# Performance work log

Hardware: AMD Instinct MI355X
Metric: run time of the kernel (lower is better)

## Reference

```python
import jax, jax.numpy as jnp
import numpy as np

DIM = 1024
NUM_HEADS = 16
HEAD_DIM = DIM // NUM_HEADS
SCALE = HEAD_DIM ** -0.5


def setup_inputs() -> dict:
    key = jax.random.key(0)
    ks = jax.random.split(key, 11)
    B, T = 2, 2048
    std = DIM ** -0.5
    return {
        "query": jax.random.normal(ks[0], (B, T, DIM), jnp.float32),
        "key": jax.random.normal(ks[1], (B, T, DIM), jnp.float32),
        "value": jax.random.normal(ks[2], (B, T, DIM), jnp.float32),
        "wq": jax.random.normal(ks[3], (DIM, DIM), jnp.float32) * std,
        "bq": jnp.zeros((DIM,), jnp.float32),
        "wk": jax.random.normal(ks[4], (DIM, DIM), jnp.float32) * std,
        "bk": jnp.zeros((DIM,), jnp.float32),
        "wv": jax.random.normal(ks[5], (DIM, DIM), jnp.float32) * std,
        "bv": jnp.zeros((DIM,), jnp.float32),
        "wo": jax.random.normal(ks[6], (DIM, DIM), jnp.float32) * std,
        "bo": jnp.zeros((DIM,), jnp.float32),
    }


def reference(query, key, value, wq, bq, wk, bk, wv, bv, wo, bo):
    B, Tq, D = query.shape
    Tk = key.shape[1]
    H, Hd = NUM_HEADS, HEAD_DIM
    # projections (torch Linear: x @ W^T + b); reshape to [B, H, T, Hd]
    q = (query @ wq.T + bq).reshape(B, Tq, H, Hd).transpose(0, 2, 1, 3)
    k = (key @ wk.T + bk).reshape(B, Tk, H, Hd).transpose(0, 2, 1, 3)
    v = (value @ wv.T + bv).reshape(B, Tk, H, Hd).transpose(0, 2, 1, 3)
    # attention scores [B, H, Tq, Tk]
    attn = jnp.einsum("bhqd,bhkd->bhqk", q, k) * SCALE
    attn = jax.nn.softmax(attn, axis=-1)
    # dropout p=0.0 -> identity
    out = jnp.einsum("bhqk,bhkd->bhqd", attn, v)
    out = out.transpose(0, 2, 1, 3).reshape(B, Tq, D)
    return out @ wo.T + bo
```

## Files before the change

kernel.cpp:

```cpp
#include <hip/hip_runtime.h>
#include <math.h>


typedef __attribute__((ext_vector_type(8))) short short8;
typedef __attribute__((ext_vector_type(4))) float f32x4;
typedef __attribute__((ext_vector_type(4))) float float4v;
typedef __attribute__((ext_vector_type(4))) unsigned short ushort4v;
typedef __attribute__((ext_vector_type(2))) unsigned int uint2v;

typedef __attribute__((address_space(3))) unsigned int lds_uint;
typedef __attribute__((address_space(1))) unsigned int glb_uint;

__device__ __forceinline__ void gload_lds16(const void* g, void* l) {
    __builtin_amdgcn_global_load_lds((glb_uint*)(unsigned long long)g,
                                     (lds_uint*)(unsigned int)(unsigned long long)l,
                                     16, 0, 0);
}

__device__ __forceinline__ unsigned short f32_bf16(float f) {
    union { float f; unsigned int u; } x; x.f = f;
    unsigned int r = x.u + 0x7fffu + ((x.u >> 16) & 1u);
    return (unsigned short)(r >> 16);
}

__device__ __forceinline__ unsigned int cvt_pk_bf16(float lo, float hi) {
    unsigned int r;
    asm("v_cvt_pk_bf16_f32 %0, %1, %2" : "=v"(r) : "v"(lo), "v"(hi));
    return r;
}

__device__ __forceinline__ float exp2_fast(float x) {
    float r;
    asm("v_exp_f32 %0, %1" : "=v"(r) : "v"(x));
    return r;
}

#define QSCALE 0.18033688011112042f

__global__ void pack3_bf16(const float* __restrict__ a, const float* __restrict__ b,
                           const float* __restrict__ c,
                           unsigned short* __restrict__ oa, unsigned short* __restrict__ ob,
                           unsigned short* __restrict__ oc, int n4) {
    const int y = blockIdx.y;
    const float* in = (y == 0) ? a : (y == 1) ? b : c;
    unsigned short* out = (y == 0) ? oa : (y == 1) ? ob : oc;
    int i = blockIdx.x * blockDim.x + threadIdx.x;
    if (i < n4) {
        float4v v = ((const float4v*)in)[i];
        ushort4v o;
        o.x = f32_bf16(v.x); o.y = f32_bf16(v.y);
        o.z = f32_bf16(v.z); o.w = f32_bf16(v.w);
        ((ushort4v*)out)[i] = o;
    }
}

__global__ void pack4_bf16(const float* __restrict__ a, const float* __restrict__ b,
                           const float* __restrict__ c, const float* __restrict__ d,
                           unsigned short* __restrict__ oa, unsigned short* __restrict__ ob,
                           unsigned short* __restrict__ oc, unsigned short* __restrict__ od,
                           int n4) {
    const int y = blockIdx.y;
    const float* in = (y == 0) ? a : (y == 1) ? b : (y == 2) ? c : d;
    unsigned short* out = (y == 0) ? oa : (y == 1) ? ob : (y == 2) ? oc : od;
    int i = blockIdx.x * blockDim.x + threadIdx.x;
    if (i < n4) {
        float4v v = ((const float4v*)in)[i];
        ushort4v o;
        o.x = f32_bf16(v.x); o.y = f32_bf16(v.y);
        o.z = f32_bf16(v.z); o.w = f32_bf16(v.w);
        ((ushort4v*)out)[i] = o;
    }
}

__global__ __launch_bounds__(256, 2) void gemm_qkv(
    const unsigned short* __restrict__ A0, const unsigned short* __restrict__ A1,
    const unsigned short* __restrict__ A2,
    const unsigned short* __restrict__ W0, const unsigned short* __restrict__ W1,
    const unsigned short* __restrict__ W2,
    const float* __restrict__ bs0, const float* __restrict__ bs1,
    const float* __restrict__ bs2,
    unsigned short* __restrict__ O0, unsigned short* __restrict__ O1,
    unsigned short* __restrict__ O2)
{
    const int z = blockIdx.z;
    const unsigned short* A = (z == 0) ? A0 : (z == 1) ? A1 : A2;
    const unsigned short* W = (z == 0) ? W0 : (z == 1) ? W1 : W2;
    const float* bias        = (z == 0) ? bs0 : (z == 1) ? bs1 : bs2;
    unsigned short* C        = (z == 0) ? O0 : (z == 1) ? O1 : O2;
    const float oscale = (z == 0) ? QSCALE : 1.0f;
    const int N = 1024, K = 1024;

    __shared__ unsigned short As[128 * 64];
    __shared__ unsigned short Bs[128 * 64];
    const int tid  = threadIdx.x;
    const int lane = tid & 63, wave = tid >> 6;
    const int l15 = lane & 15, l4 = lane >> 4;
    const int bm = blockIdx.y * 128, bn = blockIdx.x * 128;
    const int wr = wave >> 1, wc = wave & 1;

    f32x4 acc[4][4];
    #pragma unroll
    for (int i = 0; i < 4; ++i)
        #pragma unroll
        for (int j = 0; j < 4; ++j)
            #pragma unroll
            for (int e = 0; e < 4; ++e) acc[i][j][e] = 0.f;

    const int srow = lane >> 3;
    const int scol = (lane & 7) * 8;

    for (int k0 = 0; k0 < K; k0 += 64) {
        __syncthreads();
        #pragma unroll
        for (int i = 0; i < 4; ++i) {
            int c = wave * 4 + i;
            int row = c * 8 + srow;
            gload_lds16(A + (size_t)(bm + row) * K + k0 + scol, &As[c * 512]);
            gload_lds16(W + (size_t)(bn + row) * K + k0 + scol, &Bs[c * 512]);
        }
        __syncthreads();
        #pragma unroll
        for (int kk = 0; kk < 2; ++kk) {
            short8 af[4], bf[4];
            const int ko = kk * 32 + l4 * 8;
            #pragma unroll
            for (int i = 0; i < 4; ++i)
                af[i] = *(const short8*)&As[(wr * 64 + i * 16 + l15) * 64 + ko];
            #pragma unroll
            for (int j = 0; j < 4; ++j)
                bf[j] = *(const short8*)&Bs[(wc * 64 + j * 16 + l15) * 64 + ko];
            #pragma unroll
            for (int i = 0; i < 4; ++i)
                #pragma unroll
                for (int j = 0; j < 4; ++j)
                    acc[i][j] = __builtin_amdgcn_mfma_f32_16x16x32_bf16(
                        af[i], bf[j], acc[i][j], 0, 0, 0);
        }
    }

    #pragma unroll
    for (int j = 0; j < 4; ++j) {
        const int col = bn + wc * 64 + j * 16 + l15;
        const float bj = bias[col];
        #pragma unroll
        for (int i = 0; i < 4; ++i) {
            const int row0 = bm + wr * 64 + i * 16 + l4 * 4;
            #pragma unroll
            for (int r = 0; r < 4; ++r) {
                const int row = row0 + r;
                const float v = (acc[i][j][r] + bj) * oscale;
                if (z < 2) {
                    C[(size_t)row * N + col] = f32_bf16(v);
                } else {
                    const int b = row >> 11, t = row & 2047;
                    C[(((size_t)((b << 4) + (col >> 6)) * 64
                        + (col & 63)) << 11) + t] = f32_bf16(v);
                }
            }
        }
    }
}

__global__ __launch_bounds__(256, 2) void gemm_out(
    const unsigned short* __restrict__ A,
    const unsigned short* __restrict__ W,
    const float* __restrict__ bias,
    float* __restrict__ C)
{
    const int N = 1024, K = 1024;
    __shared__ unsigned short As[128 * 64];
    __shared__ unsigned short Bs[128 * 64];
    const int tid  = threadIdx.x;
    const int lane = tid & 63, wave = tid >> 6;
    const int l15 = lane & 15, l4 = lane >> 4;
    const int bm = blockIdx.y * 128, bn = blockIdx.x * 128;
    const int wr = wave >> 1, wc = wave & 1;

    f32x4 acc[4][4];
    #pragma unroll
    for (int i = 0; i < 4; ++i)
        #pragma unroll
        for (int j = 0; j < 4; ++j)
            #pragma unroll
            for (int e = 0; e < 4; ++e) acc[i][j][e] = 0.f;

    const int srow = lane >> 3;
    const int scol = (lane & 7) * 8;

    for (int k0 = 0; k0 < K; k0 += 64) {
        __syncthreads();
        #pragma unroll
        for (int i = 0; i < 4; ++i) {
            int c = wave * 4 + i;
            int row = c * 8 + srow;
            gload_lds16(A + (size_t)(bm + row) * K + k0 + scol, &As[c * 512]);
            gload_lds16(W + (size_t)(bn + row) * K + k0 + scol, &Bs[c * 512]);
        }
        __syncthreads();
        #pragma unroll
        for (int kk = 0; kk < 2; ++kk) {
            short8 af[4], bf[4];
            const int ko = kk * 32 + l4 * 8;
            #pragma unroll
            for (int i = 0; i < 4; ++i)
                af[i] = *(const short8*)&As[(wr * 64 + i * 16 + l15) * 64 + ko];
            #pragma unroll
            for (int j = 0; j < 4; ++j)
                bf[j] = *(const short8*)&Bs[(wc * 64 + j * 16 + l15) * 64 + ko];
            #pragma unroll
            for (int i = 0; i < 4; ++i)
                #pragma unroll
                for (int j = 0; j < 4; ++j)
                    acc[i][j] = __builtin_amdgcn_mfma_f32_16x16x32_bf16(
                        af[i], bf[j], acc[i][j], 0, 0, 0);
        }
    }

    #pragma unroll
    for (int j = 0; j < 4; ++j) {
        const int col = bn + wc * 64 + j * 16 + l15;
        const float bj = bias[col];
        #pragma unroll
        for (int i = 0; i < 4; ++i) {
            const int row0 = bm + wr * 64 + i * 16 + l4 * 4;
            #pragma unroll
            for (int r = 0; r < 4; ++r)
                C[(size_t)(row0 + r) * N + col] = acc[i][j][r] + bj;
        }
    }
}

__global__ __launch_bounds__(256, 4) void attn_fwd(
    const unsigned short* __restrict__ qp,
    const unsigned short* __restrict__ kp,
    const unsigned short* __restrict__ vt,
    unsigned short* __restrict__ op)
{
    __shared__ unsigned short Ks[2][64 * 64];
    __shared__ unsigned short Vs[2][64 * 64];
    __shared__ unsigned short P[4][16 * 64];

    const int tid = threadIdx.x;
    const int lane = tid & 63, wave = tid >> 6;
    const int l15 = lane & 15, l4 = lane >> 4;
    const int swz = (l15 & 7) << 3;

    const int flat = blockIdx.y * 32 + blockIdx.x;
    const int swzb = (flat & 7) * 128 + (flat >> 3);
    const int bx = swzb & 31;
    const int bh = swzb >> 5;
    const int b = bh >> 4, h = bh & 15;
    const int q0 = bx * 64 + wave * 16;

    const size_t xbase = (size_t)b * 2048 * 1024 + h * 64;
    const size_t vbase = (size_t)bh * 64 * 2048;

    const int sr = lane >> 3;
    const int sc = ((lane & 7) ^ sr) * 8;

    short8 bq[2];
    #pragma unroll
    for (int kk = 0; kk < 2; ++kk)
        bq[kk] = *(const short8*)&qp[xbase
            + (size_t)(q0 + l15) * 1024 + kk * 32 + l4 * 8];

    f32x4 acc[4];
    #pragma unroll
    for (int dj = 0; dj < 4; ++dj)
        #pragma unroll
        for (int e = 0; e < 4; ++e) acc[dj][e] = 0.f;

    float m_run = -1e30f, l_run = 0.f;

    {
        const int c0 = wave * 2;
        #pragma unroll
        for (int i = 0; i < 2; ++i) {
            const int c = c0 + i;
            gload_lds16(kp + xbase + (size_t)(c * 8 + sr) * 1024 + sc,
                        &Ks[0][c * 512]);
            gload_lds16(vt + vbase + (size_t)(c * 8 + sr) * 2048 + sc,
                        &Vs[0][c * 512]);
        }
    }
    __syncthreads();

    const int NT = 2048 / 64;
    int buf = 0;
    for (int t = 0; t < NT; ++t) {
        const int kv0 = t * 64;
        if (t + 1 < NT) {
            const int c0 = wave * 2;
            #pragma unroll
            for (int i = 0; i < 2; ++i) {
                const int c = c0 + i;
                gload_lds16(kp + xbase + (size_t)(kv0 + 64 + c * 8 + sr) * 1024 + sc,
                            &Ks[buf ^ 1][c * 512]);
                gload_lds16(vt + vbase + (size_t)(c * 8 + sr) * 2048 + kv0 + 64 + sc,
                            &Vs[buf ^ 1][c * 512]);
            }
        }

        f32x4 st[4];
        {
            short8 ak[4];
            #pragma unroll
            for (int j = 0; j < 4; ++j)
                ak[j] = *(const short8*)&Ks[buf][(j * 16 + l15) * 64
                                                 + (((0 * 4 + l4) << 3) ^ swz)];
            const f32x4 z4 = {0.f, 0.f, 0.f, 0.f};
            #pragma unroll
            for (int j = 0; j < 4; ++j)
                st[j] = __builtin_amdgcn_mfma_f32_16x16x32_bf16(
                    ak[j], bq[0], z4, 0, 0, 0);
            #pragma unroll
            for (int j = 0; j < 4; ++j)
                ak[j] = *(const short8*)&Ks[buf][(j * 16 + l15) * 64
                                                 + (((1 * 4 + l4) << 3) ^ swz)];
            #pragma unroll
            for (int j = 0; j < 4; ++j)
                st[j] = __builtin_amdgcn_mfma_f32_16x16x32_bf16(
                    ak[j], bq[1], st[j], 0, 0, 0);
        }

        short8 av[2][4];
        #pragma unroll
        for (int kvc = 0; kvc < 2; ++kvc)
            #pragma unroll
            for (int dj = 0; dj < 4; ++dj)
                av[kvc][dj] = *(const short8*)&Vs[buf][(dj * 16 + l15) * 64
                                                 + (((kvc * 4 + l4) << 3) ^ swz)];

        {
            float tm[4];
            #pragma unroll
            for (int j = 0; j < 4; ++j)
                tm[j] = fmaxf(fmaxf(st[j][0], st[j][1]),
                              fmaxf(st[j][2], st[j][3]));
            float mx = fmaxf(fmaxf(tm[0], tm[1]), fmaxf(tm[2], tm[3]));
            mx = fmaxf(mx, __shfl_xor(mx, 16));
            mx = fmaxf(mx, __shfl_xor(mx, 32));
            const float mnew = fmaxf(m_run, mx);
            const float corr = exp2_fast(m_run - mnew);
            m_run = mnew;
            float ts[4];
            #pragma unroll
            for (int j = 0; j < 4; ++j) {
                float p0 = exp2_fast(st[j][0] - mnew);
                float p1 = exp2_fast(st[j][1] - mnew);
                float p2 = exp2_fast(st[j][2] - mnew);
                float p3 = exp2_fast(st[j][3] - mnew);
                st[j][0] = p0; st[j][1] = p1; st[j][2] = p2; st[j][3] = p3;
                ts[j] = (p0 + p1) + (p2 + p3);
            }
            float ls = (ts[0] + ts[1]) + (ts[2] + ts[3]);
            ls += __shfl_xor(ls, 16);
            ls += __shfl_xor(ls, 32);
            l_run = l_run * corr + ls;
            #pragma unroll
            for (int dj = 0; dj < 4; ++dj) acc[dj] *= corr;
        }

        #pragma unroll
        for (int j = 0; j < 4; ++j) {
            uint2v w;
            w.x = cvt_pk_bf16(st[j][0], st[j][1]);
            w.y = cvt_pk_bf16(st[j][2], st[j][3]);
            *(uint2v*)&P[wave][l15 * 64 + ((j * 16 + l4 * 4) ^ swz)] = w;
        }

        #pragma unroll
        for (int kvc = 0; kvc < 2; ++kvc) {
            short8 pb = *(const short8*)&P[wave][l15 * 64
                                                + (((kvc * 4 + l4) << 3) ^ swz)];
            #pragma unroll
            for (int dj = 0; dj < 4; ++dj)
                acc[dj] = __builtin_amdgcn_mfma_f32_16x16x32_bf16(
                    av[kvc][dj], pb, acc[dj], 0, 0, 0);
        }

        __syncthreads();
        buf ^= 1;
    }

    {
        const float inv = 1.0f / l_run;
        const int t = q0 + l15;
        #pragma unroll
        for (int dj = 0; dj < 4; ++dj) {
            uint2v w;
            w.x = cvt_pk_bf16(acc[dj][0] * inv, acc[dj][1] * inv);
            w.y = cvt_pk_bf16(acc[dj][2] * inv, acc[dj][3] * inv);
            *(uint2v*)&op[((size_t)(b * 2048 + t)) * 1024
                          + h * 64 + dj * 16 + l4 * 4] = w;
        }
    }
}

extern "C" void kernel_launch(void* const* d_in, const int* in_sizes, int n_in,
                              void* d_out, int out_size, void* d_ws, size_t ws_size,
                              hipStream_t stream)
{
    const float* q  = (const float*)d_in[0];
    const float* k  = (const float*)d_in[1];
    const float* v  = (const float*)d_in[2];
    const float* wq = (const float*)d_in[3];
    const float* bq = (const float*)d_in[4];
    const float* wk = (const float*)d_in[5];
    const float* bk = (const float*)d_in[6];
    const float* wv = (const float*)d_in[7];
    const float* bv = (const float*)d_in[8];
    const float* wo = (const float*)d_in[9];
    const float* bo = (const float*)d_in[10];
    float* out = (float*)d_out;

    const int M = 4096, N = 1024, K = 1024;
    unsigned char* ws = (unsigned char*)d_ws;
    const size_t SX = (size_t)M * K * 2;
    const size_t SW = (size_t)N * K * 2;
    unsigned short* xq  = (unsigned short*)(ws);
    unsigned short* xk  = (unsigned short*)(ws + SX);
    unsigned short* xv  = (unsigned short*)(ws + 2 * SX);
    unsigned short* wqb = (unsigned short*)(ws + 3 * SX);
    unsigned short* wkb = (unsigned short*)(ws + 3 * SX + SW);
    unsigned short* wvb = (unsigned short*)(ws + 3 * SX + 2 * SW);
    unsigned short* wob = (unsigned short*)(ws + 3 * SX + 3 * SW);
    unsigned short* qp  = (unsigned short*)(ws + 3 * SX + 4 * SW);
    unsigned short* kp  = qp + (size_t)M * N;
    unsigned short* vt  = kp + (size_t)M * N;
    unsigned short* opb = vt + (size_t)M * N;

    pack3_bf16<<<dim3(4096, 3), 256, 0, stream>>>(q, k, v, xq, xk, xv,
                                                  M * K / 4);
    pack4_bf16<<<dim3(1024, 4), 256, 0, stream>>>(wq, wk, wv, wo,
                                                  wqb, wkb, wvb, wob, N * K / 4);

    gemm_qkv<<<dim3(8, 32, 3), 256, 0, stream>>>(xq, xk, xv, wqb, wkb, wvb,
                                                 bq, bk, bv, qp, kp, vt);

    attn_fwd<<<dim3(32, 32), 256, 0, stream>>>(qp, kp, vt, opb);

    gemm_out<<<dim3(8, 32), 256, 0, stream>>>(opb, wob, bo, out);
}
```

Baseline: 150.2 us.

## Double-buffer LDS staging in QKV and output GEMMs, shrink output tile

Both projection GEMMs now use two LDS buffers, issuing the async global-to-LDS load for the next K-slice before computing on the current one, with a single barrier per iteration instead of two. The output GEMM also drops to a 64x128 block tile with a doubled grid and a higher occupancy hint, giving more blocks for the 256-CU device. The aim is to hide global load latency behind MFMA work and improve occupancy on the small output GEMM. The cost is doubled LDS use in gemm_qkv, which may reduce resident blocks. The prefetch is issued without a wait before compute, so correctness depends on the barrier at the end of each iteration making the async loads visible.

```diff
diff --git a/kernel.cpp b/kernel.cpp
--- a/kernel.cpp
+++ b/kernel.cpp
@@ -90,8 +90,8 @@
     const float oscale = (z == 0) ? QSCALE : 1.0f;
     const int N = 1024, K = 1024;
 
-    __shared__ unsigned short As[128 * 64];
-    __shared__ unsigned short Bs[128 * 64];
+    __shared__ unsigned short As[2][128 * 64];
+    __shared__ unsigned short Bs[2][128 * 64];
     const int tid  = threadIdx.x;
     const int lane = tid & 63, wave = tid >> 6;
     const int l15 = lane & 15, l4 = lane >> 4;
@@ -109,26 +109,32 @@
     const int srow = lane >> 3;
     const int scol = (lane & 7) * 8;
 
+    auto stage = [&](int bf, int k0) {
+        #pragma unroll
+        for (int i = 0; i < 4; ++i) {
+            const int c = wave * 4 + i;
+            const int row = c * 8 + srow;
+            gload_lds16(A + (size_t)(bm + row) * K + k0 + scol, &As[bf][c * 512]);
+            gload_lds16(W + (size_t)(bn + row) * K + k0 + scol, &Bs[bf][c * 512]);
+        }
+    };
+
+    stage(0, 0);
+    __syncthreads();
+
+    int bufi = 0;
     for (int k0 = 0; k0 < K; k0 += 64) {
-        __syncthreads();
-        #pragma unroll
-        for (int i = 0; i < 4; ++i) {
-            int c = wave * 4 + i;
-            int row = c * 8 + srow;
-            gload_lds16(A + (size_t)(bm + row) * K + k0 + scol, &As[c * 512]);
-            gload_lds16(W + (size_t)(bn + row) * K + k0 + scol, &Bs[c * 512]);
-        }
-        __syncthreads();
+        if (k0 + 64 < K) stage(bufi ^ 1, k0 + 64);
         #pragma unroll
         for (int kk = 0; kk < 2; ++kk) {
             short8 af[4], bf[4];
             const int ko = kk * 32 + l4 * 8;
             #pragma unroll
             for (int i = 0; i < 4; ++i)
-                af[i] = *(const short8*)&As[(wr * 64 + i * 16 + l15) * 64 + ko];
-            #pragma unroll
-            for (int j = 0; j < 4; ++j)
-                bf[j] = *(const short8*)&Bs[(wc * 64 + j * 16 + l15) * 64 + ko];
+                af[i] = *(const short8*)&As[bufi][(wr * 64 + i * 16 + l15) * 64 + ko];
+            #pragma unroll
+            for (int j = 0; j < 4; ++j)
+                bf[j] = *(const short8*)&Bs[bufi][(wc * 64 + j * 16 + l15) * 64 + ko];
             #pragma unroll
             for (int i = 0; i < 4; ++i)
                 #pragma unroll
@@ -136,6 +142,8 @@
                     acc[i][j] = __builtin_amdgcn_mfma_f32_16x16x32_bf16(
                         af[i], bf[j], acc[i][j], 0, 0, 0);
         }
+        __syncthreads();
+        bufi ^= 1;
     }
 
     #pragma unroll
@@ -161,24 +169,24 @@
     }
 }
 
-__global__ __launch_bounds__(256, 2) void gemm_out(
+__global__ __launch_bounds__(256, 3) void gemm_out(
     const unsigned short* __restrict__ A,
     const unsigned short* __restrict__ W,
     const float* __restrict__ bias,
     float* __restrict__ C)
 {
     const int N = 1024, K = 1024;
-    __shared__ unsigned short As[128 * 64];
-    __shared__ unsigned short Bs[128 * 64];
+    __shared__ unsigned short As[2][64 * 64];
+    __shared__ unsigned short Bs[2][128 * 64];
     const int tid  = threadIdx.x;
     const int lane = tid & 63, wave = tid >> 6;
     const int l15 = lane & 15, l4 = lane >> 4;
-    const int bm = blockIdx.y * 128, bn = blockIdx.x * 128;
+    const int bm = blockIdx.y * 64, bn = blockIdx.x * 128;
     const int wr = wave >> 1, wc = wave & 1;
 
-    f32x4 acc[4][4];
-    #pragma unroll
-    for (int i = 0; i < 4; ++i)
+    f32x4 acc[2][4];
+    #pragma unroll
+    for (int i = 0; i < 2; ++i)
         #pragma unroll
         for (int j = 0; j < 4; ++j)
             #pragma unroll
@@ -187,33 +195,46 @@
     const int srow = lane >> 3;
     const int scol = (lane & 7) * 8;
 
+    auto stage = [&](int bf, int k0) {
+        #pragma unroll
+        for (int i = 0; i < 2; ++i) {
+            const int c = wave * 2 + i;
+            gload_lds16(A + (size_t)(bm + c * 8 + srow) * K + k0 + scol,
+                        &As[bf][c * 512]);
+        }
+        #pragma unroll
+        for (int i = 0; i < 4; ++i) {
+            const int c = wave * 4 + i;
+            gload_lds16(W + (size_t)(bn + c * 8 + srow) * K + k0 + scol,
+                        &Bs[bf][c * 512]);
+        }
+    };
+
+    stage(0, 0);
+    __syncthreads();
+
+    int bufi = 0;
     for (int k0 = 0; k0 < K; k0 += 64) {
-        __syncthreads();
-        #pragma unroll
-        for (int i = 0; i < 4; ++i) {
-            int c = wave * 4 + i;
-            int row = c * 8 + srow;
-            gload_lds16(A + (size_t)(bm + row) * K + k0 + scol, &As[c * 512]);
-            gload_lds16(W + (size_t)(bn + row) * K + k0 + scol, &Bs[c * 512]);
-        }
-        __syncthreads();
+        if (k0 + 64 < K) stage(bufi ^ 1, k0 + 64);
         #pragma unroll
         for (int kk = 0; kk < 2; ++kk) {
-            short8 af[4], bf[4];
+            short8 af[2], bf[4];
             const int ko = kk * 32 + l4 * 8;
             #pragma unroll
-            for (int i = 0; i < 4; ++i)
-                af[i] = *(const short8*)&As[(wr * 64 + i * 16 + l15) * 64 + ko];
-            #pragma unroll
-            for (int j = 0; j < 4; ++j)
-                bf[j] = *(const short8*)&Bs[(wc * 64 + j * 16 + l15) * 64 + ko];
-            #pragma unroll
-            for (int i = 0; i < 4; ++i)
+            for (int i = 0; i < 2; ++i)
+                af[i] = *(const short8*)&As[bufi][(wr * 32 + i * 16 + l15) * 64 + ko];
+            #pragma unroll
+            for (int j = 0; j < 4; ++j)
+                bf[j] = *(const short8*)&Bs[bufi][(wc * 64 + j * 16 + l15) * 64 + ko];
+            #pragma unroll
+            for (int i = 0; i < 2; ++i)
                 #pragma unroll
                 for (int j = 0; j < 4; ++j)
                     acc[i][j] = __builtin_amdgcn_mfma_f32_16x16x32_bf16(
                         af[i], bf[j], acc[i][j], 0, 0, 0);
         }
+        __syncthreads();
+        bufi ^= 1;
     }
 
     #pragma unroll
@@ -221,8 +242,8 @@
         const int col = bn + wc * 64 + j * 16 + l15;
         const float bj = bias[col];
         #pragma unroll
-        for (int i = 0; i < 4; ++i) {
-            const int row0 = bm + wr * 64 + i * 16 + l4 * 4;
+        for (int i = 0; i < 2; ++i) {
+            const int row0 = bm + wr * 32 + i * 16 + l4 * 4;
             #pragma unroll
             for (int r = 0; r < 4; ++r)
                 C[(size_t)(row0 + r) * N + col] = acc[i][j][r] + bj;
@@ -440,5 +461,5 @@
 
     attn_fwd<<<dim3(32, 32), 256, 0, stream>>>(qp, kp, vt, opb);
 
-    gemm_out<<<dim3(8, 32), 256, 0, stream>>>(opb, wob, bo, out);
-}
+    gemm_out<<<dim3(8, 64), 256, 0, stream>>>(opb, wob, bo, out);
+}
```

Result: no change. 152.7 us (+1.7%).
